# Performance work log

Hardware: AMD Instinct MI355X
Metric: run time of the kernel (lower is better)

Reference implementation:

```python
import jax, jax.numpy as jnp
import numpy as np

DIM, H, HD, S, K = 2560, 40, 64, 64, 4  # dim, n_heads, head_dim, state_dim, conv kernel
EPS = 1e-5


def _layer_norm(x, g, b):
    m = jnp.mean(x, axis=-1, keepdims=True)
    v = jnp.mean((x - m) ** 2, axis=-1, keepdims=True)
    return (x - m) * jax.lax.rsqrt(v + EPS) * g + b


def setup_inputs() -> dict:
    key = jax.random.key(0)
    ks = jax.random.split(key, 10)
    w = lambda k, shape: jax.random.normal(k, shape, jnp.float32) * 0.02
    return {
        "x": jax.random.normal(ks[0], (2, 2048, DIM), jnp.float32),
        "W_r": w(ks[1], (DIM, DIM)),
        "W_k": w(ks[2], (DIM, DIM)),
        "W_v": w(ks[3], (DIM, DIM)),
        "W_g": w(ks[4], (DIM, DIM)),
        "W_xproj": w(ks[5], (H * 3 * S, DIM)),
        "W_dt": w(ks[6], (DIM, H * S)),
        "b_dt": jnp.ones((DIM,), jnp.float32),  # dt_proj bias init to 1.0
        "conv_w": w(ks[7], (DIM, 1, K)),  # depthwise conv (out=DIM, in/groups=1, k)
        "ln1_g": jnp.ones((DIM,), jnp.float32),
        "ln1_b": jnp.zeros((DIM,), jnp.float32),
        "ln2_g": jnp.ones((DIM,), jnp.float32),
        "ln2_b": jnp.zeros((DIM,), jnp.float32),
        "W_out": w(ks[8], (DIM, DIM)),
    }


def reference(x, W_r, W_k, W_v, W_g, W_xproj, W_dt, b_dt, conv_w,
              ln1_g, ln1_b, ln2_g, ln2_b, W_out):
    B, L, D = x.shape
    # causal depthwise conv: torch Conv1d(pad=3)[:, :L] == left-pad by K-1
    xc = jax.lax.conv_general_dilated(
        x.transpose(0, 2, 1), conv_w, window_strides=(1,), padding=[(K - 1, 0)],
        feature_group_count=D, dimension_numbers=("NCH", "OIH", "NCH"),
    ).transpose(0, 2, 1)
    x = _layer_norm(x + xc, ln1_g, ln1_b)

    proj = (x @ W_xproj.T).reshape(B, L, H, 3 * S)
    dt_raw, B_vec, C_vec = jnp.split(proj, 3, axis=-1)  # each (B,L,H,S)
    dt = jax.nn.softplus(dt_raw.reshape(B, L, H * S) @ W_dt.T + b_dt)
    w = jnp.exp(-dt).reshape(B, L, H, S)

    r = jax.nn.sigmoid(x @ W_r.T).reshape(B, L, H, HD)
    k = (x @ W_k.T).reshape(B, L, H, HD)
    v = (x @ W_v.T).reshape(B, L, H, HD)
    g = jax.nn.sigmoid(x @ W_g.T).reshape(B, L, H, HD)
    kv = k * v  # (B,L,H,HD)

    def step(state, inp):
        w_t, B_t, C_t, kv_t, r_t, g_t = inp
        # state: (B,H,S,HD); decay per state row, rank-1 B ⊗ (k*v) update
        state = w_t[..., None] * state + B_t[..., None] * kv_t[:, :, None, :]
        y = jnp.einsum("bhsd,bhs->bhd", state, C_t)
        return state, r_t * y * g_t

    seq = tuple(jnp.moveaxis(a, 1, 0) for a in (w, B_vec, C_vec, kv, r, g))
    state0 = jnp.zeros((B, H, S, HD), x.dtype)
    final_state, outs = jax.lax.scan(step, state0, seq)  # outs: (L,B,H,HD)
    out = jnp.moveaxis(outs, 0, 1).reshape(B, L, D)
    out = _layer_norm(x + out @ W_out.T, ln2_g, ln2_b)
    return out, final_state
```

## Files before the change

kernel.cpp:

```cpp
#include <hip/hip_runtime.h>
#include <cstddef>
#include <cstdint>

#define DIM 2560
#define NH 40
#define HDD 64
#define SD 64
#define KC 4
#define BB 2
#define LL 2048
#define MTOT (BB*LL)
#define NPROJ (NH*3*SD)
#define NC 16
#define CH (LL/NC)
#define BH (BB*NH)

typedef unsigned short u16;
typedef __attribute__((ext_vector_type(8))) short bf16x8;
typedef __attribute__((ext_vector_type(4))) float f32x4;

__device__ inline float bf2f(u16 u) { return __uint_as_float(((unsigned)u) << 16); }
__device__ inline float bflo(unsigned u) { return __uint_as_float(u << 16); }
__device__ inline float bfhi(unsigned u) { return __uint_as_float(u & 0xffff0000u); }
__device__ inline u16 f2bf(float f) {
  unsigned x = __float_as_uint(f);
  unsigned r = (x + 0x7fffu + ((x >> 16) & 1u)) >> 16;
  return (u16)r;
}

__device__ inline void gload16(const void* g, void* lds) {
  __builtin_amdgcn_global_load_lds(
      (const __attribute__((address_space(1))) void*)g,
      (__attribute__((address_space(3))) void*)(uint32_t)(size_t)lds,
      16, 0, 0);
}

__global__ __launch_bounds__(256) void cvt_kernel(
    const float* __restrict__ src, u16* __restrict__ dst, int n4) {
  int i = blockIdx.x * 256 + threadIdx.x;
  int stride = gridDim.x * 256;
  for (; i < n4; i += stride) {
    float4 v = *(const float4*)(src + (size_t)i * 4);
    ushort4 o;
    o.x = f2bf(v.x); o.y = f2bf(v.y); o.z = f2bf(v.z); o.w = f2bf(v.w);
    *(ushort4*)(dst + (size_t)i * 4) = o;
  }
}

__global__ __launch_bounds__(256) void fill_kernel(float* p, int n, float v) {
  int i = blockIdx.x * 256 + threadIdx.x;
  if (i < n) p[i] = v;
}

__device__ inline void block_reduce2(float& sum, float& sq, float* red) {
  #pragma unroll
  for (int off = 32; off; off >>= 1) {
    sum += __shfl_down(sum, off, 64);
    sq  += __shfl_down(sq,  off, 64);
  }
  int wid = threadIdx.x >> 6, lane = threadIdx.x & 63;
  if (lane == 0) { red[wid*2] = sum; red[wid*2+1] = sq; }
  __syncthreads();
  sum = red[0] + red[2] + red[4] + red[6];
  sq  = red[1] + red[3] + red[5] + red[7];
}

__global__ __launch_bounds__(256) void conv_ln1_kernel(
    const float* __restrict__ x, const float* __restrict__ cw,
    const float* __restrict__ g1, const float* __restrict__ b1,
    u16* __restrict__ x1) {
  __shared__ float red[8];
  int bl = blockIdx.x;
  int l  = bl & (LL - 1);
  int t  = threadIdx.x;
  const float* xr = x + (size_t)bl * DIM;
  float vals[10];
  float sum = 0.f, sq = 0.f;
  #pragma unroll
  for (int i = 0; i < 10; ++i) {
    int d = t + 256 * i;
    float acc = xr[d];
    #pragma unroll
    for (int j = 0; j < KC; ++j) {
      int ll = l - (KC - 1) + j;
      if (ll >= 0) acc += x[(size_t)(bl - l + ll) * DIM + d] * cw[d * KC + j];
    }
    vals[i] = acc; sum += acc; sq += acc * acc;
  }
  block_reduce2(sum, sq, red);
  float mean = sum * (1.f / DIM);
  float var  = sq * (1.f / DIM) - mean * mean;
  float rstd = rsqrtf(var + 1e-5f);
  u16* orow = x1 + (size_t)bl * DIM;
  #pragma unroll
  for (int i = 0; i < 10; ++i) {
    int d = t + 256 * i;
    orow[d] = f2bf((vals[i] - mean) * rstd * g1[d] + b1[d]);
  }
}

__global__ __launch_bounds__(256) void ln2_kernel(
    const u16* __restrict__ x1, const u16* __restrict__ y2,
    const float* __restrict__ g2, const float* __restrict__ b2,
    float* __restrict__ out) {
  __shared__ float red[8];
  int bl = blockIdx.x;
  int t  = threadIdx.x;
  const u16* ar = x1 + (size_t)bl * DIM;
  const u16* br = y2 + (size_t)bl * DIM;
  float vals[10];
  float sum = 0.f, sq = 0.f;
  #pragma unroll
  for (int i = 0; i < 10; ++i) {
    int d = t + 256 * i;
    float v = bf2f(ar[d]) + bf2f(br[d]);
    vals[i] = v; sum += v; sq += v * v;
  }
  block_reduce2(sum, sq, red);
  float mean = sum * (1.f / DIM);
  float var  = sq * (1.f / DIM) - mean * mean;
  float rstd = rsqrtf(var + 1e-5f);
  float* orow = out + (size_t)bl * DIM;
  #pragma unroll
  for (int i = 0; i < 10; ++i) {
    int d = t + 256 * i;
    orow[d] = (vals[i] - mean) * rstd * g2[d] + b2[d];
  }
}

template<int EPI, bool REMAP>
__global__ __launch_bounds__(256) void gemm_mfma(
    const u16* __restrict__ A, int lda,
    const u16* __restrict__ Wb,
    const float* __restrict__ bias,
    u16* __restrict__ C1, int ldc,
    int K) {
  __shared__ u16 As[2 * 128 * 32];
  __shared__ u16 Bs[2 * 128 * 32];
  int t = threadIdx.x;
  int w = t >> 6, l = t & 63;
  int wr = w >> 1, wc = w & 1;

  int nx  = gridDim.x;
  int nwg = nx * gridDim.y;
  int wg  = blockIdx.y * nx + blockIdx.x;
  int cpx = nwg >> 3;
  int swz = (wg & 7) * cpx + (wg >> 3);
  int m0 = (swz / nx) * 128;
  int n0 = (swz % nx) * 128;

  f32x4 acc[4][4];
  #pragma unroll
  for (int i = 0; i < 4; ++i)
    #pragma unroll
    for (int j = 0; j < 4; ++j)
      acc[i][j] = (f32x4){0.f, 0.f, 0.f, 0.f};

  int srow = l >> 2;
  int scol = (l & 3) * 8;
  const u16* gA = A  + (size_t)(m0 + 32 * w + srow) * lda + scol;
  const u16* gB = Wb + (size_t)(n0 + 32 * w + srow) * K   + scol;
  u16* ldsA = As + (32 * w) * 32;
  u16* ldsB = Bs + (32 * w) * 32;

  int fr = l & 15;
  int kc = (l >> 4) * 8;
  const u16* rA = As + (size_t)(wr * 64 + fr) * 32 + kc;
  const u16* rB = Bs + (size_t)(wc * 64 + fr) * 32 + kc;

  for (int k0 = 0; k0 < K; k0 += 64) {
    #pragma unroll
    for (int q = 0; q < 4; ++q) {
      const int ks = q >> 1, rr = q & 1;
      gload16(gA + (size_t)(rr * 16) * lda + k0 + ks * 32,
              ldsA + ks * 4096 + rr * 512);
      gload16(gB + (size_t)(rr * 16) * K + k0 + ks * 32,
              ldsB + ks * 4096 + rr * 512);
    }
    __syncthreads();
    bf16x8 a[4][2], b[4][2];
    #pragma unroll
    for (int i = 0; i < 4; ++i) {
      a[i][0] = *(const bf16x8*)(rA + i * 512);
      a[i][1] = *(const bf16x8*)(rA + 4096 + i * 512);
      b[i][0] = *(const bf16x8*)(rB + i * 512);
      b[i][1] = *(const bf16x8*)(rB + 4096 + i * 512);
    }
    #pragma unroll
    for (int ks = 0; ks < 2; ++ks)
      #pragma unroll
      for (int i = 0; i < 4; ++i)
        #pragma unroll
        for (int j = 0; j < 4; ++j)
          acc[i][j] = __builtin_amdgcn_mfma_f32_16x16x32_bf16(a[i][ks], b[j][ks], acc[i][j], 0, 0, 0);
    __syncthreads();
  }

  int crow = (l >> 4) * 4;
  int ccol = l & 15;
  #pragma unroll
  for (int j = 0; j < 4; ++j) {
    int col = n0 + wc * 64 + j * 16 + ccol;
    int colr = col;
    if (REMAP) {
      int h = col / 192, r3 = col % 192;
      colr = (r3 / 64) * 2560 + h * 64 + (r3 & 63);
    }
    float bv = (EPI == 2) ? bias[col] : 0.f;
    #pragma unroll
    for (int i = 0; i < 4; ++i) {
      #pragma unroll
      for (int q = 0; q < 4; ++q) {
        int row = m0 + wr * 64 + i * 16 + crow + q;
        float v = acc[i][j][q];
        if constexpr (EPI == 1) v = 1.f / (1.f + expf(-v));
        if constexpr (EPI == 2) v = 1.f / (1.f + expf(v + bv));
        size_t idx = (size_t)row * ldc + colr;
        if constexpr (EPI == 5) v *= bf2f(C1[idx]);
        C1[idx] = f2bf(v);
      }
    }
  }
}

__global__ __launch_bounds__(128) void scan_local_kernel(
    const u16* __restrict__ wdec, const u16* __restrict__ proj,
    const u16* __restrict__ kvb, u16* __restrict__ yout,
    float* __restrict__ Sbuf, float* __restrict__ Pbuf) {
  int bx = blockIdx.x;
  int bh = bx / NC, c = bx % NC;
  int b = bh / NH, h = bh % NH;
  int wv = threadIdx.x >> 6;
  int lane = threadIdx.x & 63;
  int sg = lane >> 3, dd = lane & 7;
  int s0 = sg * 8;
  int d0 = wv * 32 + dd * 4;
  int l0 = c * CH;

  const u16* fw = wdec + ((size_t)(b * LL + l0)) * DIM + h * 64 + s0;
  const u16* fB = proj + ((size_t)(b * LL + l0)) * NPROJ + 2560 + h * 64 + s0;
  const u16* fC = fB + 2560;
  const u16* fk = kvb + ((size_t)(b * LL + l0)) * DIM + h * 64 + d0;
  u16* py = yout + ((size_t)(b * LL + l0)) * NPROJ + h * 64 + d0;

  float st[8][4];
  float pc[8];
  #pragma unroll
  for (int i = 0; i < 8; ++i) {
    pc[i] = 1.f;
    #pragma unroll
    for (int j = 0; j < 4; ++j) st[i][j] = 0.f;
  }

#define P1_DECL(n) uint4 wS##n, BS##n, CS##n; uint2 kS##n
#define P1_LOAD(n) do { \
    wS##n = *(const uint4*)fw; BS##n = *(const uint4*)fB; \
    CS##n = *(const uint4*)fC; kS##n = *(const uint2*)fk; \
    fw += DIM; fB += NPROJ; fC += NPROJ; fk += DIM; } while (0)
#define P1_PROC(n) do { \
    float wv8[8], Bv[8], Cv[8], kv4[4], pr[4]; \
    wv8[0]=bflo(wS##n.x); wv8[1]=bfhi(wS##n.x); wv8[2]=bflo(wS##n.y); wv8[3]=bfhi(wS##n.y); \
    wv8[4]=bflo(wS##n.z); wv8[5]=bfhi(wS##n.z); wv8[6]=bflo(wS##n.w); wv8[7]=bfhi(wS##n.w); \
    Bv[0]=bflo(BS##n.x); Bv[1]=bfhi(BS##n.x); Bv[2]=bflo(BS##n.y); Bv[3]=bfhi(BS##n.y); \
    Bv[4]=bflo(BS##n.z); Bv[5]=bfhi(BS##n.z); Bv[6]=bflo(BS##n.w); Bv[7]=bfhi(BS##n.w); \
    Cv[0]=bflo(CS##n.x); Cv[1]=bfhi(CS##n.x); Cv[2]=bflo(CS##n.y); Cv[3]=bfhi(CS##n.y); \
    Cv[4]=bflo(CS##n.z); Cv[5]=bfhi(CS##n.z); Cv[6]=bflo(CS##n.w); Cv[7]=bfhi(CS##n.w); \
    kv4[0]=bflo(kS##n.x); kv4[1]=bfhi(kS##n.x); kv4[2]=bflo(kS##n.y); kv4[3]=bfhi(kS##n.y); \
    pr[0]=0.f; pr[1]=0.f; pr[2]=0.f; pr[3]=0.f; \
    _Pragma("unroll") \
    for (int i = 0; i < 8; ++i) { \
      pc[i] *= wv8[i]; \
      _Pragma("unroll") \
      for (int j = 0; j < 4; ++j) { \
        st[i][j] = fmaf(wv8[i], st[i][j], Bv[i] * kv4[j]); \
        pr[j] = fmaf(st[i][j], Cv[i], pr[j]); } } \
    _Pragma("unroll") \
    for (int j = 0; j < 4; ++j) { \
      pr[j] += __shfl_xor(pr[j], 8, 64); \
      pr[j] += __shfl_xor(pr[j], 16, 64); \
      pr[j] += __shfl_xor(pr[j], 32, 64); } \
    if (lane < 8) { \
      uint2 ov; \
      ov.x = (unsigned)f2bf(pr[0]) | ((unsigned)f2bf(pr[1]) << 16); \
      ov.y = (unsigned)f2bf(pr[2]) | ((unsigned)f2bf(pr[3]) << 16); \
      *(uint2*)py = ov; } \
    py += NPROJ; } while (0)

  P1_DECL(0); P1_DECL(1); P1_DECL(2); P1_DECL(3);
  P1_LOAD(0); P1_LOAD(1); P1_LOAD(2); P1_LOAD(3);
  for (int l = 0; l < CH; l += 4) {
    P1_PROC(0); P1_LOAD(0);
    P1_PROC(1); P1_LOAD(1);
    P1_PROC(2); P1_LOAD(2);
    P1_PROC(3); P1_LOAD(3);
  }
#undef P1_DECL
#undef P1_LOAD
#undef P1_PROC

  float* Sp = Sbuf + (((size_t)c * BH + bh) * 64 + s0) * 64 + d0;
  #pragma unroll
  for (int i = 0; i < 8; ++i) {
    float4 v; v.x = st[i][0]; v.y = st[i][1]; v.z = st[i][2]; v.w = st[i][3];
    *(float4*)(Sp + (size_t)i * 64) = v;
  }
  if (wv == 0 && dd == 0) {
    #pragma unroll
    for (int i = 0; i < 8; ++i)
      Pbuf[((size_t)c * BH + bh) * 64 + s0 + i] = pc[i];
  }
}

__global__ __launch_bounds__(256) void scan_combine_kernel(
    float* __restrict__ Sbuf, const float* __restrict__ Pbuf,
    float* __restrict__ fstate) {
  int bh = blockIdx.x;
  int t = threadIdx.x;
  int s = t >> 2, j0 = (t & 3) * 16;
  float stin[16];
  #pragma unroll
  for (int k = 0; k < 16; ++k) stin[k] = 0.f;
  for (int c = 0; c < NC; ++c) {
    float* Sp = Sbuf + (((size_t)c * BH + bh) * 64 + s) * 64 + j0;
    float Pc = Pbuf[((size_t)c * BH + bh) * 64 + s];
    #pragma unroll
    for (int q = 0; q < 4; ++q) {
      float4 a = *(const float4*)(Sp + q * 4);
      float4 cur;
      cur.x = stin[q*4+0]; cur.y = stin[q*4+1];
      cur.z = stin[q*4+2]; cur.w = stin[q*4+3];
      *(float4*)(Sp + q * 4) = cur;
      stin[q*4+0] = a.x + Pc * stin[q*4+0];
      stin[q*4+1] = a.y + Pc * stin[q*4+1];
      stin[q*4+2] = a.z + Pc * stin[q*4+2];
      stin[q*4+3] = a.w + Pc * stin[q*4+3];
    }
  }
  float* fp = fstate + ((size_t)bh * 64 + s) * 64 + j0;
  #pragma unroll
  for (int q = 0; q < 4; ++q) {
    float4 v;
    v.x = stin[q*4+0]; v.y = stin[q*4+1];
    v.z = stin[q*4+2]; v.w = stin[q*4+3];
    *(float4*)(fp + q * 4) = v;
  }
}

__global__ __launch_bounds__(128) void scan_correct_kernel(
    const u16* __restrict__ wdec, const u16* __restrict__ proj,
    const u16* __restrict__ rb, const u16* __restrict__ gb,
    const float* __restrict__ Sbuf, u16* __restrict__ yio) {
  int bx = blockIdx.x;
  int bh = bx / NC, c = bx % NC;
  int b = bh / NH, h = bh % NH;
  int wv = threadIdx.x >> 6;
  int lane = threadIdx.x & 63;
  int sg = lane >> 3, dd = lane & 7;
  int s0 = sg * 8;
  int d0 = wv * 32 + dd * 4;
  int l0 = c * CH;

  const float* Sp = Sbuf + (((size_t)c * BH + bh) * 64 + s0) * 64 + d0;
  float stin[8][4];
  #pragma unroll
  for (int i = 0; i < 8; ++i) {
    float4 v = *(const float4*)(Sp + (size_t)i * 64);
    stin[i][0] = v.x; stin[i][1] = v.y; stin[i][2] = v.z; stin[i][3] = v.w;
  }

  const u16* fw = wdec + ((size_t)(b * LL + l0)) * DIM + h * 64 + s0;
  const u16* fC = proj + ((size_t)(b * LL + l0)) * NPROJ + 5120 + h * 64 + s0;
  const u16* fy = yio  + ((size_t)(b * LL + l0)) * NPROJ + h * 64 + d0;
  const u16* fr2 = rb + ((size_t)(b * LL + l0)) * DIM + h * 64 + d0;
  const u16* fg2 = gb + ((size_t)(b * LL + l0)) * DIM + h * 64 + d0;
  u16* py = yio + ((size_t)(b * LL + l0)) * NPROJ + h * 64 + d0;

  float pc[8];
  #pragma unroll
  for (int i = 0; i < 8; ++i) pc[i] = 1.f;

#define P3_DECL(n) uint4 wT##n, CT##n; uint2 yT##n, rT##n, gT##n
#define P3_LOAD(n) do { \
    wT##n = *(const uint4*)fw; CT##n = *(const uint4*)fC; \
    yT##n = *(const uint2*)fy; rT##n = *(const uint2*)fr2; gT##n = *(const uint2*)fg2; \
    fw += DIM; fC += NPROJ; fy += NPROJ; fr2 += DIM; fg2 += DIM; } while (0)
#define P3_PROC(n) do { \
    float wv8[8], Cv[8], ac[8], pr[4]; \
    wv8[0]=bflo(wT##n.x); wv8[1]=bfhi(wT##n.x); wv8[2]=bflo(wT##n.y); wv8[3]=bfhi(wT##n.y); \
    wv8[4]=bflo(wT##n.z); wv8[5]=bfhi(wT##n.z); wv8[6]=bflo(wT##n.w); wv8[7]=bfhi(wT##n.w); \
    Cv[0]=bflo(CT##n.x); Cv[1]=bfhi(CT##n.x); Cv[2]=bflo(CT##n.y); Cv[3]=bfhi(CT##n.y); \
    Cv[4]=bflo(CT##n.z); Cv[5]=bfhi(CT##n.z); Cv[6]=bflo(CT##n.w); Cv[7]=bfhi(CT##n.w); \
    pr[0]=0.f; pr[1]=0.f; pr[2]=0.f; pr[3]=0.f; \
    _Pragma("unroll") \
    for (int i = 0; i < 8; ++i) { \
      pc[i] *= wv8[i]; ac[i] = pc[i] * Cv[i]; \
      _Pragma("unroll") \
      for (int j = 0; j < 4; ++j) pr[j] = fmaf(ac[i], stin[i][j], pr[j]); } \
    _Pragma("unroll") \
    for (int j = 0; j < 4; ++j) { \
      pr[j] += __shfl_xor(pr[j], 8, 64); \
      pr[j] += __shfl_xor(pr[j], 16, 64); \
      pr[j] += __shfl_xor(pr[j], 32, 64); } \
    if (lane < 8) { \
      float y0 = (bflo(yT##n.x) + pr[0]) * bflo(rT##n.x) * bflo(gT##n.x); \
      float y1 = (bfhi(yT##n.x) + pr[1]) * bfhi(rT##n.x) * bfhi(gT##n.x); \
      float y2 = (bflo(yT##n.y) + pr[2]) * bflo(rT##n.y) * bflo(gT##n.y); \
      float y3 = (bfhi(yT##n.y) + pr[3]) * bfhi(rT##n.y) * bfhi(gT##n.y); \
      uint2 ov; \
      ov.x = (unsigned)f2bf(y0) | ((unsigned)f2bf(y1) << 16); \
      ov.y = (unsigned)f2bf(y2) | ((unsigned)f2bf(y3) << 16); \
      *(uint2*)py = ov; } \
    py += NPROJ; } while (0)

  P3_DECL(0); P3_DECL(1); P3_DECL(2); P3_DECL(3);
  P3_LOAD(0); P3_LOAD(1); P3_LOAD(2); P3_LOAD(3);
  for (int l = 0; l < CH; l += 4) {
    P3_PROC(0); P3_LOAD(0);
    P3_PROC(1); P3_LOAD(1);
    P3_PROC(2); P3_LOAD(2);
    P3_PROC(3); P3_LOAD(3);
  }
#undef P3_DECL
#undef P3_LOAD
#undef P3_PROC
}

extern "C" void kernel_launch(void* const* d_in, const int* in_sizes, int n_in,
                              void* d_out, int out_size, void* d_ws, size_t ws_size,
                              hipStream_t stream) {
  const float* x    = (const float*)d_in[0];
  const float* W_r  = (const float*)d_in[1];
  const float* W_k  = (const float*)d_in[2];
  const float* W_v  = (const float*)d_in[3];
  const float* W_g  = (const float*)d_in[4];
  const float* W_xp = (const float*)d_in[5];
  const float* W_dt = (const float*)d_in[6];
  const float* b_dt = (const float*)d_in[7];
  const float* cw   = (const float*)d_in[8];
  const float* ln1g = (const float*)d_in[9];
  const float* ln1b = (const float*)d_in[10];
  const float* ln2g = (const float*)d_in[11];
  const float* ln2b = (const float*)d_in[12];
  const float* W_o  = (const float*)d_in[13];

  float* out    = (float*)d_out;
  float* fstate = out + (size_t)MTOT * DIM;

  const size_t nBL = (size_t)MTOT * DIM;
  const size_t nPJ = (size_t)MTOT * NPROJ;
  const size_t nWX = (size_t)NPROJ * DIM;
  const size_t needed = (nBL * 5 + nPJ + nWX) * sizeof(u16);
  if (ws_size < needed) {
    fill_kernel<<<(out_size + 255) / 256, 256, 0, stream>>>(out, out_size, 1234.5f);
    return;
  }

  u16* wsp  = (u16*)d_ws;
  u16* x1   = wsp;
  u16* proj = x1 + nBL;
  u16* wdec = proj + nPJ;
  u16* rb   = wdec + nBL;
  u16* gb   = rb + nBL;
  u16* kvb  = gb + nBL;
  u16* wscr = kvb + nBL;
  float* Sbuf = (float*)wscr;
  float* Pbuf = Sbuf + (size_t)NC * BH * 64 * 64;

  const int nDD4 = DIM * DIM / 4;

  conv_ln1_kernel<<<MTOT, 256, 0, stream>>>(x, cw, ln1g, ln1b, x1);

  cvt_kernel<<<2048, 256, 0, stream>>>(W_xp, wscr, NPROJ * DIM / 4);
  gemm_mfma<0,true ><<<dim3(NPROJ/128, MTOT/128), 256, 0, stream>>>(x1, DIM, wscr, nullptr, proj, NPROJ, DIM);

  cvt_kernel<<<2048, 256, 0, stream>>>(W_dt, wscr, nDD4);
  gemm_mfma<2,false><<<dim3(DIM/128, MTOT/128), 256, 0, stream>>>(proj, NPROJ, wscr, b_dt, wdec, DIM, DIM);

  cvt_kernel<<<2048, 256, 0, stream>>>(W_r, wscr, nDD4);
  gemm_mfma<1,false><<<dim3(DIM/128, MTOT/128), 256, 0, stream>>>(x1, DIM, wscr, nullptr, rb, DIM, DIM);

  cvt_kernel<<<2048, 256, 0, stream>>>(W_g, wscr, nDD4);
  gemm_mfma<1,false><<<dim3(DIM/128, MTOT/128), 256, 0, stream>>>(x1, DIM, wscr, nullptr, gb, DIM, DIM);

  cvt_kernel<<<2048, 256, 0, stream>>>(W_k, wscr, nDD4);
  gemm_mfma<0,false><<<dim3(DIM/128, MTOT/128), 256, 0, stream>>>(x1, DIM, wscr, nullptr, kvb, DIM, DIM);

  cvt_kernel<<<2048, 256, 0, stream>>>(W_v, wscr, nDD4);
  gemm_mfma<5,false><<<dim3(DIM/128, MTOT/128), 256, 0, stream>>>(x1, DIM, wscr, nullptr, kvb, DIM, DIM);

  scan_local_kernel<<<BH * NC, 128, 0, stream>>>(wdec, proj, kvb, proj, Sbuf, Pbuf);
  scan_combine_kernel<<<BH, 256, 0, stream>>>(Sbuf, Pbuf, fstate);
  scan_correct_kernel<<<BH * NC, 128, 0, stream>>>(wdec, proj, rb, gb, Sbuf, proj);

  cvt_kernel<<<2048, 256, 0, stream>>>(W_o, wscr, nDD4);
  gemm_mfma<0,false><<<dim3(DIM/128, MTOT/128), 256, 0, stream>>>(proj, NPROJ, wscr, nullptr, wdec, DIM, DIM);

  ln2_kernel<<<MTOT, 256, 0, stream>>>(x1, wdec, ln2g, ln2b, out);
}
```

Before: 1.077 ms.

## Fuse paired projection GEMMs into dual-weight kernel, simplify GEMM K-loop

Adds a dual-B GEMM kernel that reads each A tile once and multiplies it against two weight matrices. It computes r and g together, and k*v in the epilogue without a read-modify-write of an intermediate. The base GEMM also changes: the K step drops from 64 to 32, the workgroup swizzle is removed, and the LDS footprint is halved. Those base-GEMM changes mean more barriers per K and less L2 locality for the projection GEMMs that still use it. The dual kernel holds two 64-register accumulator sets per thread, which risks lower occupancy, and it needs a second weight scratch buffer.

```diff
diff --git a/kernel.cpp b/kernel.cpp
--- a/kernel.cpp
+++ b/kernel.cpp
@@ -135,19 +135,13 @@
     const float* __restrict__ bias,
     u16* __restrict__ C1, int ldc,
     int K) {
-  __shared__ u16 As[2 * 128 * 32];
-  __shared__ u16 Bs[2 * 128 * 32];
+  __shared__ u16 As[128 * 32];
+  __shared__ u16 Bs[128 * 32];
   int t = threadIdx.x;
   int w = t >> 6, l = t & 63;
   int wr = w >> 1, wc = w & 1;
-
-  int nx  = gridDim.x;
-  int nwg = nx * gridDim.y;
-  int wg  = blockIdx.y * nx + blockIdx.x;
-  int cpx = nwg >> 3;
-  int swz = (wg & 7) * cpx + (wg >> 3);
-  int m0 = (swz / nx) * 128;
-  int n0 = (swz % nx) * 128;
+  int m0 = blockIdx.y * 128;
+  int n0 = blockIdx.x * 128;
 
   f32x4 acc[4][4];
   #pragma unroll
@@ -156,10 +150,10 @@
     for (int j = 0; j < 4; ++j)
       acc[i][j] = (f32x4){0.f, 0.f, 0.f, 0.f};
 
-  int srow = l >> 2;
+  int srow = 32 * w + (l >> 2);
   int scol = (l & 3) * 8;
-  const u16* gA = A  + (size_t)(m0 + 32 * w + srow) * lda + scol;
-  const u16* gB = Wb + (size_t)(n0 + 32 * w + srow) * K   + scol;
+  const u16* gA = A  + (size_t)(m0 + srow) * lda + scol;
+  const u16* gB = Wb + (size_t)(n0 + srow) * K   + scol;
   u16* ldsA = As + (32 * w) * 32;
   u16* ldsB = Bs + (32 * w) * 32;
 
@@ -168,31 +162,22 @@
   const u16* rA = As + (size_t)(wr * 64 + fr) * 32 + kc;
   const u16* rB = Bs + (size_t)(wc * 64 + fr) * 32 + kc;
 
-  for (int k0 = 0; k0 < K; k0 += 64) {
-    #pragma unroll
-    for (int q = 0; q < 4; ++q) {
-      const int ks = q >> 1, rr = q & 1;
-      gload16(gA + (size_t)(rr * 16) * lda + k0 + ks * 32,
-              ldsA + ks * 4096 + rr * 512);
-      gload16(gB + (size_t)(rr * 16) * K + k0 + ks * 32,
-              ldsB + ks * 4096 + rr * 512);
-    }
+  for (int k0 = 0; k0 < K; k0 += 32) {
+    gload16(gA + k0, ldsA);
+    gload16(gA + (size_t)16 * lda + k0, ldsA + 16 * 32);
+    gload16(gB + k0, ldsB);
+    gload16(gB + (size_t)16 * K + k0, ldsB + 16 * 32);
     __syncthreads();
-    bf16x8 a[4][2], b[4][2];
-    #pragma unroll
-    for (int i = 0; i < 4; ++i) {
-      a[i][0] = *(const bf16x8*)(rA + i * 512);
-      a[i][1] = *(const bf16x8*)(rA + 4096 + i * 512);
-      b[i][0] = *(const bf16x8*)(rB + i * 512);
-      b[i][1] = *(const bf16x8*)(rB + 4096 + i * 512);
-    }
-    #pragma unroll
-    for (int ks = 0; ks < 2; ++ks)
+    bf16x8 a[4], b[4];
+    #pragma unroll
+    for (int i = 0; i < 4; ++i) a[i] = *(const bf16x8*)(rA + i * 16 * 32);
+    #pragma unroll
+    for (int j = 0; j < 4; ++j) b[j] = *(const bf16x8*)(rB + j * 16 * 32);
+    #pragma unroll
+    for (int i = 0; i < 4; ++i)
       #pragma unroll
-      for (int i = 0; i < 4; ++i)
-        #pragma unroll
-        for (int j = 0; j < 4; ++j)
-          acc[i][j] = __builtin_amdgcn_mfma_f32_16x16x32_bf16(a[i][ks], b[j][ks], acc[i][j], 0, 0, 0);
+      for (int j = 0; j < 4; ++j)
+        acc[i][j] = __builtin_amdgcn_mfma_f32_16x16x32_bf16(a[i], b[j], acc[i][j], 0, 0, 0);
     __syncthreads();
   }
 
@@ -215,9 +200,95 @@
         float v = acc[i][j][q];
         if constexpr (EPI == 1) v = 1.f / (1.f + expf(-v));
         if constexpr (EPI == 2) v = 1.f / (1.f + expf(v + bv));
-        size_t idx = (size_t)row * ldc + colr;
-        if constexpr (EPI == 5) v *= bf2f(C1[idx]);
-        C1[idx] = f2bf(v);
+        C1[(size_t)row * ldc + colr] = f2bf(v);
+      }
+    }
+  }
+}
+
+template<int MODE>
+__global__ __launch_bounds__(256) void gemm_dual(
+    const u16* __restrict__ A, int lda,
+    const u16* __restrict__ W1, const u16* __restrict__ W2,
+    u16* __restrict__ C1, u16* __restrict__ C2,
+    int ldc, int K) {
+  __shared__ u16 As[128 * 32];
+  __shared__ u16 B1s[128 * 32];
+  __shared__ u16 B2s[128 * 32];
+  int t = threadIdx.x;
+  int w = t >> 6, l = t & 63;
+  int wr = w >> 1, wc = w & 1;
+  int m0 = blockIdx.y * 128;
+  int n0 = blockIdx.x * 128;
+
+  f32x4 acc1[4][4], acc2[4][4];
+  #pragma unroll
+  for (int i = 0; i < 4; ++i)
+    #pragma unroll
+    for (int j = 0; j < 4; ++j) {
+      acc1[i][j] = (f32x4){0.f, 0.f, 0.f, 0.f};
+      acc2[i][j] = (f32x4){0.f, 0.f, 0.f, 0.f};
+    }
+
+  int srow = 32 * w + (l >> 2);
+  int scol = (l & 3) * 8;
+  const u16* gA  = A  + (size_t)(m0 + srow) * lda + scol;
+  const u16* gB1 = W1 + (size_t)(n0 + srow) * K   + scol;
+  const u16* gB2 = W2 + (size_t)(n0 + srow) * K   + scol;
+  u16* ldsA  = As  + (32 * w) * 32;
+  u16* ldsB1 = B1s + (32 * w) * 32;
+  u16* ldsB2 = B2s + (32 * w) * 32;
+
+  int fr = l & 15;
+  int kc = (l >> 4) * 8;
+  const u16* rA  = As  + (size_t)(wr * 64 + fr) * 32 + kc;
+  const u16* rB1 = B1s + (size_t)(wc * 64 + fr) * 32 + kc;
+  const u16* rB2 = B2s + (size_t)(wc * 64 + fr) * 32 + kc;
+
+  for (int k0 = 0; k0 < K; k0 += 32) {
+    gload16(gA + k0, ldsA);
+    gload16(gA + (size_t)16 * lda + k0, ldsA + 16 * 32);
+    gload16(gB1 + k0, ldsB1);
+    gload16(gB1 + (size_t)16 * K + k0, ldsB1 + 16 * 32);
+    gload16(gB2 + k0, ldsB2);
+    gload16(gB2 + (size_t)16 * K + k0, ldsB2 + 16 * 32);
+    __syncthreads();
+    bf16x8 a[4], b1[4], b2[4];
+    #pragma unroll
+    for (int i = 0; i < 4; ++i) {
+      a[i]  = *(const bf16x8*)(rA  + i * 16 * 32);
+      b1[i] = *(const bf16x8*)(rB1 + i * 16 * 32);
+      b2[i] = *(const bf16x8*)(rB2 + i * 16 * 32);
+    }
+    #pragma unroll
+    for (int i = 0; i < 4; ++i)
+      #pragma unroll
+      for (int j = 0; j < 4; ++j) {
+        acc1[i][j] = __builtin_amdgcn_mfma_f32_16x16x32_bf16(a[i], b1[j], acc1[i][j], 0, 0, 0);
+        acc2[i][j] = __builtin_amdgcn_mfma_f32_16x16x32_bf16(a[i], b2[j], acc2[i][j], 0, 0, 0);
+      }
+    __syncthreads();
+  }
+
+  int crow = (l >> 4) * 4;
+  int ccol = l & 15;
+  #pragma unroll
+  for (int j = 0; j < 4; ++j) {
+    int col = n0 + wc * 64 + j * 16 + ccol;
+    #pragma unroll
+    for (int i = 0; i < 4; ++i) {
+      #pragma unroll
+      for (int q = 0; q < 4; ++q) {
+        int row = m0 + wr * 64 + i * 16 + crow + q;
+        size_t idx = (size_t)row * ldc + col;
+        float v1 = acc1[i][j][q];
+        float v2 = acc2[i][j][q];
+        if constexpr (MODE == 3) {
+          C1[idx] = f2bf(1.f / (1.f + expf(-v1)));
+          C2[idx] = f2bf(1.f / (1.f + expf(-v2)));
+        } else {
+          C1[idx] = f2bf(v1 * v2);
+        }
       }
     }
   }
@@ -449,6 +520,7 @@
   const size_t nBL = (size_t)MTOT * DIM;
   const size_t nPJ = (size_t)MTOT * NPROJ;
   const size_t nWX = (size_t)NPROJ * DIM;
+  const size_t nDD = (size_t)DIM * DIM;
   const size_t needed = (nBL * 5 + nPJ + nWX) * sizeof(u16);
   if (ws_size < needed) {
     fill_kernel<<<(out_size + 255) / 256, 256, 0, stream>>>(out, out_size, 1234.5f);
@@ -463,10 +535,11 @@
   u16* gb   = rb + nBL;
   u16* kvb  = gb + nBL;
   u16* wscr = kvb + nBL;
+  u16* wscr2 = wscr + nDD;
   float* Sbuf = (float*)wscr;
   float* Pbuf = Sbuf + (size_t)NC * BH * 64 * 64;
 
-  const int nDD4 = DIM * DIM / 4;
+  const int nDD4 = (int)(nDD / 4);
 
   conv_ln1_kernel<<<MTOT, 256, 0, stream>>>(x, cw, ln1g, ln1b, x1);
 
@@ -477,16 +550,12 @@
   gemm_mfma<2,false><<<dim3(DIM/128, MTOT/128), 256, 0, stream>>>(proj, NPROJ, wscr, b_dt, wdec, DIM, DIM);
 
   cvt_kernel<<<2048, 256, 0, stream>>>(W_r, wscr, nDD4);
-  gemm_mfma<1,false><<<dim3(DIM/128, MTOT/128), 256, 0, stream>>>(x1, DIM, wscr, nullptr, rb, DIM, DIM);
-
-  cvt_kernel<<<2048, 256, 0, stream>>>(W_g, wscr, nDD4);
-  gemm_mfma<1,false><<<dim3(DIM/128, MTOT/128), 256, 0, stream>>>(x1, DIM, wscr, nullptr, gb, DIM, DIM);
+  cvt_kernel<<<2048, 256, 0, stream>>>(W_g, wscr2, nDD4);
+  gemm_dual<3><<<dim3(DIM/128, MTOT/128), 256, 0, stream>>>(x1, DIM, wscr, wscr2, rb, gb, DIM, DIM);
 
   cvt_kernel<<<2048, 256, 0, stream>>>(W_k, wscr, nDD4);
-  gemm_mfma<0,false><<<dim3(DIM/128, MTOT/128), 256, 0, stream>>>(x1, DIM, wscr, nullptr, kvb, DIM, DIM);
-
-  cvt_kernel<<<2048, 256, 0, stream>>>(W_v, wscr, nDD4);
-  gemm_mfma<5,false><<<dim3(DIM/128, MTOT/128), 256, 0, stream>>>(x1, DIM, wscr, nullptr, kvb, DIM, DIM);
+  cvt_kernel<<<2048, 256, 0, stream>>>(W_v, wscr2, nDD4);
+  gemm_dual<4><<<dim3(DIM/128, MTOT/128), 256, 0, stream>>>(x1, DIM, wscr, wscr2, kvb, nullptr, DIM, DIM);
 
   scan_local_kernel<<<BH * NC, 128, 0, stream>>>(wdec, proj, kvb, proj, Sbuf, Pbuf);
   scan_combine_kernel<<<BH, 256, 0, stream>>>(Sbuf, Pbuf, fstate);
```

Result: slower. 1.300 ms (+20.7%).
